# Kernel optimization log

Measured on AMD Instinct MI355X. Metric: run time of the kernel, lower is better.

The kernel has to match this reference:

```python
import jax, jax.numpy as jnp
import numpy as np

D_IN = 1024
D_OUT = 1024
SEQ = 2048
BATCH = 4


def setup_inputs() -> dict:
    key = jax.random.key(0)
    ks = jax.random.split(key, 7)
    s_in = 1.0 / np.sqrt(D_IN)
    return {
        "x": jax.random.normal(ks[0], (BATCH, SEQ, D_IN), dtype=jnp.float32),
        "Wq": jax.random.normal(ks[1], (D_IN, D_OUT), dtype=jnp.float32) * s_in,
        "bq": jax.random.normal(ks[2], (D_OUT,), dtype=jnp.float32) * 0.01,
        "Wk": jax.random.normal(ks[3], (D_IN, D_OUT), dtype=jnp.float32) * s_in,
        "bk": jax.random.normal(ks[4], (D_OUT,), dtype=jnp.float32) * 0.01,
        "Wv": jax.random.normal(ks[5], (D_IN, D_OUT), dtype=jnp.float32) * s_in,
        "bv": jax.random.normal(ks[6], (D_OUT,), dtype=jnp.float32) * 0.01,
    }


def reference(x, Wq, bq, Wk, bk, Wv, bv):
    # x: [b, n, d_in]
    b, n, d_in = x.shape
    q = x @ Wq + bq  # [b, n, d_out]
    k = x @ Wk + bk
    v = x @ Wv + bv
    scale = 1.0 / jnp.sqrt(jnp.asarray(d_in, x.dtype))
    scores = jnp.einsum("bqd,bkd->bqk", q, k) * scale  # [b, n, n]
    causal = jnp.triu(jnp.ones((n, n), dtype=bool), k=1)  # True above diagonal
    scores = jnp.where(causal, -jnp.inf, scores)
    weights = jax.nn.softmax(scores, axis=-1)
    # dropout p=0.0 -> identity
    context = jnp.einsum("bqk,bkd->bqd", weights, v)
    return context
```

## Files before the change

kernel.cpp:

```cpp
#include <hip/hip_runtime.h>

typedef unsigned short u16;
typedef __bf16 bf16x8 __attribute__((ext_vector_type(8)));
typedef float floatx4 __attribute__((ext_vector_type(4)));

#define B_ 4
#define SEQ 2048
#define DIM 1024

__device__ __forceinline__ u16 f2bf(float f) {
    unsigned u = __builtin_bit_cast(unsigned, f);
    u += 0x7FFFu + ((u >> 16) & 1u);
    return (u16)(u >> 16);
}
__device__ __forceinline__ float bf2f(u16 h) {
    unsigned u = ((unsigned)h) << 16;
    return __builtin_bit_cast(float, u);
}

#define GPTR(p) ((const __attribute__((address_space(1))) void*)(p))
#define LPTR(p) ((__attribute__((address_space(3))) void*)(p))

__global__ __launch_bounds__(256) void convert_x(const float4* __restrict__ x,
                                                 ushort4* __restrict__ xb) {
    int i = blockIdx.x * 256 + threadIdx.x;
    float4 v = x[i];
    ushort4 o;
    o.x = f2bf(v.x); o.y = f2bf(v.y); o.z = f2bf(v.z); o.w = f2bf(v.w);
    xb[i] = o;
}

__global__ __launch_bounds__(256) void transpose_w(const float* __restrict__ Wq,
                                                   const float* __restrict__ Wk,
                                                   const float* __restrict__ Wv,
                                                   u16* __restrict__ Wt) {
    __shared__ u16 t[64][66];
    const int z = blockIdx.z;
    const float* W = (z == 0) ? Wq : ((z == 1) ? Wk : Wv);
    u16* out = Wt + (size_t)z * DIM * DIM;
    const int tx = threadIdx.x, ty = threadIdx.y;
    const int k0 = blockIdx.x * 64, n0 = blockIdx.y * 64;
#pragma unroll
    for (int j = 0; j < 8; j++) {
        int k = ty + 8 * j;
        float2 v = *(const float2*)(W + (size_t)(k0 + k) * DIM + n0 + 2 * tx);
        t[2 * tx][k] = f2bf(v.x);
        t[2 * tx + 1][k] = f2bf(v.y);
    }
    __syncthreads();
#pragma unroll
    for (int j = 0; j < 8; j++) {
        int n = ty + 8 * j;
        ushort2 o;
        o.x = t[n][2 * tx];
        o.y = t[n][2 * tx + 1];
        *(ushort2*)(out + (size_t)(n0 + n) * DIM + k0 + 2 * tx) = o;
    }
}

__device__ __forceinline__ void mainloop(
    const u16* __restrict__ Ab, const u16* __restrict__ Bb, int lda, int ldb,
    int Kt, u16* lsA, u16* lsB, int tid, int wave, int quad, int l15,
    int wm, int wn, floatx4 (&acc)[4][4]) {
    const int srow = tid >> 2;
    const int scol = ((tid & 3) ^ ((tid >> 3) & 3)) * 8;
    const u16* gA = Ab + (size_t)srow * lda + scol;
    const u16* gB = Bb + (size_t)srow * ldb + scol;
    const int swq = (quad ^ ((l15 >> 1) & 3)) * 8;

#pragma unroll
    for (int i = 0; i < 4; i++)
#pragma unroll
        for (int j = 0; j < 4; j++) {
            floatx4 zz = {0.f, 0.f, 0.f, 0.f};
            acc[i][j] = zz;
        }

    for (int k0 = 0; k0 < Kt; k0 += 64) {
#pragma unroll
        for (int h = 0; h < 2; h++)
#pragma unroll
            for (int c = 0; c < 2; c++) {
                __builtin_amdgcn_global_load_lds(
                    GPTR(gA + (size_t)c * 64 * lda + h * 32),
                    LPTR(lsA + h * 4096 + c * 2048 + wave * 512), 16, 0, 0);
                __builtin_amdgcn_global_load_lds(
                    GPTR(gB + (size_t)c * 64 * ldb + h * 32),
                    LPTR(lsB + h * 4096 + c * 2048 + wave * 512), 16, 0, 0);
            }
        gA += 64; gB += 64;
        __syncthreads();

#pragma unroll
        for (int h = 0; h < 2; h++) {
            bf16x8 af[4];
#pragma unroll
            for (int i = 0; i < 4; i++)
                af[i] = *(const bf16x8*)(lsA + h * 4096 + (wm + i * 16 + l15) * 32 + swq);
#pragma unroll
            for (int j = 0; j < 4; j++) {
                bf16x8 bfr = *(const bf16x8*)(lsB + h * 4096 + (wn + j * 16 + l15) * 32 + swq);
#pragma unroll
                for (int i = 0; i < 4; i++)
                    acc[i][j] = __builtin_amdgcn_mfma_f32_16x16x32_bf16(af[i], bfr, acc[i][j], 0, 0, 0);
            }
        }
        __syncthreads();
    }
}

__global__ __launch_bounds__(256, 3) void gemm_qkv(
    const u16* __restrict__ A, const u16* __restrict__ Bt, u16* __restrict__ QK,
    const float* __restrict__ b0, const float* __restrict__ b1, const float* __restrict__ b2,
    u16* __restrict__ VtOut) {
    __shared__ union {
        struct { u16 a[128 * 64]; u16 b[128 * 64]; } stage;
        u16 epT[64 * 136];
    } sm;
    const int tid = threadIdx.x;
    const int wave = tid >> 6, lane = tid & 63;
    const int quad = lane >> 4, l15 = lane & 15;
    const int wm = (wave >> 1) * 64, wn = (wave & 1) * 64;
    const int z = blockIdx.x >> 3, xn = blockIdx.x & 7, yb = blockIdx.y;

    const u16* Ab = A + (size_t)yb * 128 * DIM;
    const u16* Bb = Bt + (size_t)z * DIM * DIM + (size_t)xn * 128 * DIM;
    floatx4 acc[4][4];
    mainloop(Ab, Bb, DIM, DIM, DIM, sm.stage.a, sm.stage.b,
             tid, wave, quad, l15, wm, wn, acc);

    const int colbase = xn * 128;
    const int mq = quad * 4;
    const float* bias = (z == 0) ? b0 : ((z == 1) ? b1 : b2);
    const int n0 = colbase + wn + l15;

    if (z < 2) {
        u16* Cb = QK + (size_t)z * B_ * SEQ * DIM;
        const int m0 = yb * 128 + wm + mq;
#pragma unroll
        for (int j = 0; j < 4; j++) {
            float bv_ = bias[n0 + j * 16];
#pragma unroll
            for (int i = 0; i < 4; i++)
#pragma unroll
                for (int r = 0; r < 4; r++)
                    Cb[(size_t)(m0 + i * 16 + r) * DIM + (n0 + j * 16)] = f2bf(acc[i][j][r] + bv_);
        }
        return;
    }

    float addj[4];
#pragma unroll
    for (int j = 0; j < 4; j++) addj[j] = bias[n0 + j * 16];
    const int b = (yb * 128) >> 11;
    const int sb = (yb * 128) & (SEQ - 1);
    u16* Vb = VtOut + (size_t)b * DIM * SEQ;
#pragma unroll
    for (int c = 0; c < 2; c++) {
        __syncthreads();
        if ((wave & 1) == c) {
#pragma unroll
            for (int i = 0; i < 4; i++)
#pragma unroll
                for (int j = 0; j < 4; j++)
#pragma unroll
                    for (int r = 0; r < 4; r++) {
                        int lr = wm + i * 16 + mq + r;
                        int lc = j * 16 + l15;
                        sm.epT[lc * 136 + lr] = f2bf(acc[i][j][r] + addj[j]);
                    }
        }
        __syncthreads();
#pragma unroll
        for (int k = 0; k < 4; k++) {
            int s2 = tid + 256 * k;
            int n = s2 >> 4, seg = s2 & 15;
            uint4 val = *(const uint4*)&sm.epT[n * 136 + seg * 8];
            *(uint4*)(Vb + (size_t)(colbase + c * 64 + n) * SEQ + sb + seg * 8) = val;
        }
    }
}

__global__ __launch_bounds__(256, 3) void gemm_scores(
    const u16* __restrict__ Q, const u16* __restrict__ K, u16* __restrict__ S,
    float scale) {
    const int ym = gridDim.y - 1 - blockIdx.y;
    if ((int)blockIdx.x > ym) return;

    __shared__ u16 lsA[128 * 64];
    __shared__ u16 lsB[128 * 64];
    const int tid = threadIdx.x;
    const int wave = tid >> 6, lane = tid & 63;
    const int quad = lane >> 4, l15 = lane & 15;
    const int wm = (wave >> 1) * 64, wn = (wave & 1) * 64;
    const int z = blockIdx.z;

    const u16* Ab = Q + (size_t)z * SEQ * DIM + (size_t)ym * 128 * DIM;
    const u16* Bb = K + (size_t)z * SEQ * DIM + (size_t)blockIdx.x * 128 * DIM;
    floatx4 acc[4][4];
    mainloop(Ab, Bb, DIM, DIM, DIM, lsA, lsB,
             tid, wave, quad, l15, wm, wn, acc);

    u16* Cb = S + (size_t)z * SEQ * SEQ;
    const int m0 = ym * 128 + wm + quad * 4;
    const int n0 = blockIdx.x * 128 + wn + l15;
#pragma unroll
    for (int j = 0; j < 4; j++)
#pragma unroll
        for (int i = 0; i < 4; i++)
#pragma unroll
            for (int r = 0; r < 4; r++)
                Cb[(size_t)(m0 + i * 16 + r) * SEQ + (n0 + j * 16)] = f2bf(acc[i][j][r] * scale);
}

__global__ __launch_bounds__(256, 3) void gemm_pv(
    const u16* __restrict__ P, const u16* __restrict__ Vt, float* __restrict__ O) {
    const int ym = gridDim.y - 1 - blockIdx.y;
    __shared__ u16 lsA[128 * 64];
    __shared__ u16 lsB[128 * 64];
    const int tid = threadIdx.x;
    const int wave = tid >> 6, lane = tid & 63;
    const int quad = lane >> 4, l15 = lane & 15;
    const int wm = (wave >> 1) * 64, wn = (wave & 1) * 64;
    const int z = blockIdx.z;

    const u16* Ab = P + (size_t)z * SEQ * SEQ + (size_t)ym * 128 * SEQ;
    const u16* Bb = Vt + (size_t)z * DIM * SEQ + (size_t)blockIdx.x * 128 * SEQ;
    const int Kt = (ym + 1) * 128;
    floatx4 acc[4][4];
    mainloop(Ab, Bb, SEQ, SEQ, Kt, lsA, lsB,
             tid, wave, quad, l15, wm, wn, acc);

    float* Cf = O + (size_t)z * SEQ * DIM;
    const int m0 = ym * 128 + wm + quad * 4;
    const int n0 = blockIdx.x * 128 + wn + l15;
#pragma unroll
    for (int j = 0; j < 4; j++)
#pragma unroll
        for (int i = 0; i < 4; i++)
#pragma unroll
            for (int r = 0; r < 4; r++)
                Cf[(size_t)(m0 + i * 16 + r) * DIM + (n0 + j * 16)] = acc[i][j][r];
}

__global__ __launch_bounds__(256) void softmax_causal(u16* __restrict__ S) {
    const int q = blockIdx.x, b = blockIdx.y, tid = threadIdx.x;
    u16* row = S + ((size_t)b * SEQ + q) * SEQ;
    const int L = q + 1;
    const int Z = ((q >> 7) + 1) << 7;
    const int k0 = tid * 8;
    __shared__ float redm[4], reds[4];

    uint4 rv = ((const uint4*)row)[tid];
    unsigned w[4] = {rv.x, rv.y, rv.z, rv.w};
    float f[8];
#pragma unroll
    for (int e = 0; e < 8; e++) {
        u16 h = (u16)((w[e >> 1] >> ((e & 1) * 16)) & 0xFFFFu);
        f[e] = (k0 + e < L) ? bf2f(h) : -3.0e38f;
    }
    float m = f[0];
#pragma unroll
    for (int e = 1; e < 8; e++) m = fmaxf(m, f[e]);
#pragma unroll
    for (int o = 32; o > 0; o >>= 1) m = fmaxf(m, __shfl_xor(m, o));
    if ((tid & 63) == 0) redm[tid >> 6] = m;
    __syncthreads();
    m = fmaxf(fmaxf(redm[0], redm[1]), fmaxf(redm[2], redm[3]));

    float p[8];
    float s = 0.f;
#pragma unroll
    for (int e = 0; e < 8; e++) {
        p[e] = (k0 + e < L) ? __expf(f[e] - m) : 0.f;
        s += p[e];
    }
#pragma unroll
    for (int o = 32; o > 0; o >>= 1) s += __shfl_xor(s, o);
    if ((tid & 63) == 0) reds[tid >> 6] = s;
    __syncthreads();
    s = reds[0] + reds[1] + reds[2] + reds[3];
    const float inv = 1.0f / s;

    if (k0 < Z) {
        unsigned o2[4];
#pragma unroll
        for (int e = 0; e < 4; e++) {
            unsigned lo = f2bf(p[2 * e] * inv);
            unsigned hi = f2bf(p[2 * e + 1] * inv);
            o2[e] = lo | (hi << 16);
        }
        uint4 ov = {o2[0], o2[1], o2[2], o2[3]};
        ((uint4*)row)[tid] = ov;
    }
}

extern "C" void kernel_launch(void* const* d_in, const int* in_sizes, int n_in,
                              void* d_out, int out_size, void* d_ws, size_t ws_size,
                              hipStream_t stream) {
    const float* x = (const float*)d_in[0];
    const float* Wq = (const float*)d_in[1];
    const float* bq = (const float*)d_in[2];
    const float* Wk = (const float*)d_in[3];
    const float* bk = (const float*)d_in[4];
    const float* Wv = (const float*)d_in[5];
    const float* bv = (const float*)d_in[6];
    float* out = (float*)d_out;

    char* ws = (char*)d_ws;
    const size_t MB = 1024ull * 1024ull;
    u16* S = (u16*)ws;
    u16* xb = (u16*)ws;
    u16* Wt = (u16*)(ws + 16 * MB);
    u16* QK = (u16*)(ws + 32 * MB);
    u16* Vt = (u16*)(ws + 64 * MB);
    const size_t MAT = (size_t)B_ * SEQ * DIM;
    u16* Q = QK;
    u16* Km = QK + MAT;

    const float scale = 0.03125f;

    convert_x<<<8192, 256, 0, stream>>>((const float4*)x, (ushort4*)xb);
    transpose_w<<<dim3(16, 16, 3), dim3(32, 8), 0, stream>>>(Wq, Wk, Wv, Wt);
    gemm_qkv<<<dim3(24, 64), 256, 0, stream>>>(xb, Wt, QK, bq, bk, bv, Vt);
    gemm_scores<<<dim3(16, 16, 4), 256, 0, stream>>>(Q, Km, S, scale);
    softmax_causal<<<dim3(SEQ, B_), 256, 0, stream>>>(S);
    gemm_pv<<<dim3(8, 16, 4), 256, 0, stream>>>(S, Vt, out);
}
```

Before: 250.7 us.

## Rewrite QKV projection GEMM with 256x256 tiles and pipelined direct-to-LDS loads

Replaces the 128x128-tile QKV GEMM with a 512-thread kernel computing 256x256 tiles. It double-buffers operands in LDS using global_load_lds, with staggered waitcnt/barrier phases so prefetch overlaps MFMA work. Workgroups are remapped so tiles sharing operands are scheduled close together, and the V transpose epilogue now uses an XOR-swizzled LDS buffer. The larger tile raises data reuse and cuts global traffic. The cost is 128KB of LDS and heavy register use, which lowers occupancy and leaves 384 blocks for the GPU's compute units.

```diff
diff --git a/kernel.cpp b/kernel.cpp
--- a/kernel.cpp
+++ b/kernel.cpp
@@ -20,6 +20,7 @@
 
 #define GPTR(p) ((const __attribute__((address_space(1))) void*)(p))
 #define LPTR(p) ((__attribute__((address_space(3))) void*)(p))
+#define GLD(src, dstp) __builtin_amdgcn_global_load_lds(GPTR(src), LPTR(dstp), 16, 0, 0)
 
 __global__ __launch_bounds__(256) void convert_x(const float4* __restrict__ x,
                                                  ushort4* __restrict__ xb) {
@@ -109,75 +110,172 @@
     }
 }
 
-__global__ __launch_bounds__(256, 3) void gemm_qkv(
+__global__ __launch_bounds__(512, 2) void gemm_qkv256(
     const u16* __restrict__ A, const u16* __restrict__ Bt, u16* __restrict__ QK,
     const float* __restrict__ b0, const float* __restrict__ b1, const float* __restrict__ b2,
     u16* __restrict__ VtOut) {
     __shared__ union {
-        struct { u16 a[128 * 64]; u16 b[128 * 64]; } stage;
-        u16 epT[64 * 136];
+        u16 stage[2][32768];
+        u16 T[65536];
     } sm;
+    u16* lsbase = &sm.stage[0][0];
+
     const int tid = threadIdx.x;
     const int wave = tid >> 6, lane = tid & 63;
     const int quad = lane >> 4, l15 = lane & 15;
-    const int wm = (wave >> 1) * 64, wn = (wave & 1) * 64;
-    const int z = blockIdx.x >> 3, xn = blockIdx.x & 7, yb = blockIdx.y;
-
-    const u16* Ab = A + (size_t)yb * 128 * DIM;
-    const u16* Bb = Bt + (size_t)z * DIM * DIM + (size_t)xn * 128 * DIM;
-    floatx4 acc[4][4];
-    mainloop(Ab, Bb, DIM, DIM, DIM, sm.stage.a, sm.stage.b,
-             tid, wave, quad, l15, wm, wn, acc);
-
-    const int colbase = xn * 128;
-    const int mq = quad * 4;
+    const int wmH = wave >> 2;
+    const int wnI = wave & 3;
+    const int swq = (quad ^ ((l15 >> 1) & 3)) * 8;
+    const int rdoff = l15 * 32 + swq;
+
+    const int bid = blockIdx.x;
+    const int wgid = (bid & 7) * 48 + (bid >> 3);
+    const int mt = wgid & 31, nt = wgid >> 5;
+
+    const int rl = (tid & 255) >> 2;
+    const int sS = tid >> 8;
+    const int sseg = ((tid & 3) ^ ((tid >> 3) & 3)) * 8;
+    const u16* sA = A + (size_t)mt * 256 * DIM + (size_t)rl * DIM + sS * 32 + sseg;
+    const u16* sB = Bt + (size_t)nt * 256 * DIM + (size_t)rl * DIM + sS * 32 + sseg;
+
+    {
+        u16* An0 = lsbase;
+        u16* Bn0 = lsbase + 16384;
+        GLD(sB,                      Bn0 + 0     + wave * 512);
+        GLD(sB + (size_t)64  * DIM,  Bn0 + 4096  + wave * 512);
+        GLD(sB + (size_t)128 * DIM,  Bn0 + 8192  + wave * 512);
+        GLD(sB + (size_t)192 * DIM,  Bn0 + 12288 + wave * 512);
+        GLD(sA,                      An0 + 0     + wave * 512);
+        GLD(sA + (size_t)128 * DIM,  An0 + 8192  + wave * 512);
+        GLD(sA + (size_t)64  * DIM,  An0 + 4096  + wave * 512);
+        GLD(sA + (size_t)192 * DIM,  An0 + 12288 + wave * 512);
+    }
+    const u16* sAk = sA + 64;
+    const u16* sBk = sB + 64;
+
+    floatx4 acc[8][4];
+#pragma unroll
+    for (int i = 0; i < 8; i++)
+#pragma unroll
+        for (int j = 0; j < 4; j++) {
+            floatx4 zz = {0.f, 0.f, 0.f, 0.f};
+            acc[i][j] = zz;
+        }
+
+    const int NT = DIM / 64;
+#pragma unroll 2
+    for (int t = 0; t < NT; ++t) {
+        const u16* Ac = lsbase + (t & 1) * 32768 + wmH * 8192;
+        const u16* Bc = lsbase + (t & 1) * 32768 + 16384 + (wnI >> 1) * 8192 + (wnI & 1) * 4096;
+        u16* An = lsbase + ((t & 1) ^ 1) * 32768;
+        u16* Bn = An + 16384;
+        const bool pf = (t + 1 < NT);
+        bf16x8 bq[4][2];
+
+#pragma unroll
+        for (int p = 0; p < 4; ++p) {
+            if (p == 0)       asm volatile("s_waitcnt vmcnt(2)" ::: "memory");
+            else if (p == 2) {
+                if (pf)       asm volatile("s_waitcnt vmcnt(4)" ::: "memory");
+                else          asm volatile("s_waitcnt vmcnt(0)" ::: "memory");
+            }
+            else if (p == 1)  asm volatile("s_waitcnt vmcnt(4)" ::: "memory");
+            else              asm volatile("s_waitcnt vmcnt(6)" ::: "memory");
+            __builtin_amdgcn_s_barrier();
+            asm volatile("" ::: "memory");
+
+            if (pf) {
+                if (p == 0) {
+                    GLD(sBk,                      Bn + 0     + wave * 512);
+                    GLD(sBk + (size_t)64  * DIM,  Bn + 4096  + wave * 512);
+                } else if (p == 1) {
+                    GLD(sBk + (size_t)128 * DIM,  Bn + 8192  + wave * 512);
+                    GLD(sBk + (size_t)192 * DIM,  Bn + 12288 + wave * 512);
+                } else if (p == 2) {
+                    GLD(sAk,                      An + 0     + wave * 512);
+                    GLD(sAk + (size_t)128 * DIM,  An + 8192  + wave * 512);
+                } else {
+                    GLD(sAk + (size_t)64  * DIM,  An + 4096  + wave * 512);
+                    GLD(sAk + (size_t)192 * DIM,  An + 12288 + wave * 512);
+                }
+            }
+
+            if (p == 0) {
+#pragma unroll
+                for (int j = 0; j < 4; ++j)
+#pragma unroll
+                    for (int s = 0; s < 2; ++s)
+                        bq[j][s] = *(const bf16x8*)(Bc + s * 2048 + j * 512 + rdoff);
+            }
+            const int i0 = 2 * p, i1 = 2 * p + 1;
+            bf16x8 a0[2], a1[2];
+#pragma unroll
+            for (int s = 0; s < 2; ++s) {
+                a0[s] = *(const bf16x8*)(Ac + (i0 >> 2) * 4096 + s * 2048 + (i0 & 3) * 512 + rdoff);
+                a1[s] = *(const bf16x8*)(Ac + (i1 >> 2) * 4096 + s * 2048 + (i1 & 3) * 512 + rdoff);
+            }
+
+            __builtin_amdgcn_s_setprio(1);
+#pragma unroll
+            for (int s = 0; s < 2; ++s)
+#pragma unroll
+                for (int j = 0; j < 4; ++j) {
+                    acc[i0][j] = __builtin_amdgcn_mfma_f32_16x16x32_bf16(a0[s], bq[j][s], acc[i0][j], 0, 0, 0);
+                    acc[i1][j] = __builtin_amdgcn_mfma_f32_16x16x32_bf16(a1[s], bq[j][s], acc[i1][j], 0, 0, 0);
+                }
+            __builtin_amdgcn_s_setprio(0);
+        }
+        if (pf) { sAk += 64; sBk += 64; }
+    }
+
+    const int z = nt >> 2;
+    const int nc = (nt & 3) * 256 + wnI * 64 + l15;
     const float* bias = (z == 0) ? b0 : ((z == 1) ? b1 : b2);
-    const int n0 = colbase + wn + l15;
 
     if (z < 2) {
         u16* Cb = QK + (size_t)z * B_ * SEQ * DIM;
-        const int m0 = yb * 128 + wm + mq;
-#pragma unroll
-        for (int j = 0; j < 4; j++) {
-            float bv_ = bias[n0 + j * 16];
-#pragma unroll
-            for (int i = 0; i < 4; i++)
-#pragma unroll
-                for (int r = 0; r < 4; r++)
-                    Cb[(size_t)(m0 + i * 16 + r) * DIM + (n0 + j * 16)] = f2bf(acc[i][j][r] + bv_);
+        const int m00 = mt * 256 + wmH * 128 + quad * 4;
+#pragma unroll
+        for (int j = 0; j < 4; ++j) {
+            float bv_ = bias[nc + j * 16];
+#pragma unroll
+            for (int i = 0; i < 8; ++i)
+#pragma unroll
+                for (int r = 0; r < 4; ++r)
+                    Cb[(size_t)(m00 + i * 16 + r) * DIM + nc + j * 16] =
+                        f2bf(acc[i][j][r] + bv_);
         }
         return;
     }
 
     float addj[4];
 #pragma unroll
-    for (int j = 0; j < 4; j++) addj[j] = bias[n0 + j * 16];
-    const int b = (yb * 128) >> 11;
-    const int sb = (yb * 128) & (SEQ - 1);
-    u16* Vb = VtOut + (size_t)b * DIM * SEQ;
-#pragma unroll
-    for (int c = 0; c < 2; c++) {
-        __syncthreads();
-        if ((wave & 1) == c) {
-#pragma unroll
-            for (int i = 0; i < 4; i++)
-#pragma unroll
-                for (int j = 0; j < 4; j++)
-#pragma unroll
-                    for (int r = 0; r < 4; r++) {
-                        int lr = wm + i * 16 + mq + r;
-                        int lc = j * 16 + l15;
-                        sm.epT[lc * 136 + lr] = f2bf(acc[i][j][r] + addj[j]);
-                    }
-        }
-        __syncthreads();
-#pragma unroll
-        for (int k = 0; k < 4; k++) {
-            int s2 = tid + 256 * k;
-            int n = s2 >> 4, seg = s2 & 15;
-            uint4 val = *(const uint4*)&sm.epT[n * 136 + seg * 8];
-            *(uint4*)(Vb + (size_t)(colbase + c * 64 + n) * SEQ + sb + seg * 8) = val;
-        }
+    for (int j = 0; j < 4; ++j) addj[j] = bias[nc + j * 16];
+    __syncthreads();
+#pragma unroll
+    for (int i = 0; i < 8; ++i) {
+        const int tb = wmH * 128 + i * 16 + quad * 4;
+#pragma unroll
+        for (int j = 0; j < 4; ++j) {
+            const int d = wnI * 64 + j * 16 + l15;
+            ushort4 o;
+            o.x = f2bf(acc[i][j][0] + addj[j]);
+            o.y = f2bf(acc[i][j][1] + addj[j]);
+            o.z = f2bf(acc[i][j][2] + addj[j]);
+            o.w = f2bf(acc[i][j][3] + addj[j]);
+            *(ushort4*)&sm.T[d * 256 + (tb ^ ((d & 7) << 3))] = o;
+        }
+    }
+    __syncthreads();
+    const int bI = mt >> 3;
+    const int sbase = (mt & 7) * 256;
+    u16* Vb = VtOut + (size_t)bI * DIM * SEQ + (size_t)(nt - 8) * 256 * SEQ + sbase;
+#pragma unroll
+    for (int k = 0; k < 16; ++k) {
+        int idx = tid + 512 * k;
+        int d = idx >> 5, sg = idx & 31;
+        uint4 v = *(const uint4*)&sm.T[d * 256 + ((sg * 8) ^ ((d & 7) << 3))];
+        *(uint4*)(Vb + (size_t)d * SEQ + sg * 8) = v;
     }
 }
 
@@ -322,7 +420,7 @@
 
     convert_x<<<8192, 256, 0, stream>>>((const float4*)x, (ushort4*)xb);
     transpose_w<<<dim3(16, 16, 3), dim3(32, 8), 0, stream>>>(Wq, Wk, Wv, Wt);
-    gemm_qkv<<<dim3(24, 64), 256, 0, stream>>>(xb, Wt, QK, bq, bk, bv, Vt);
+    gemm_qkv256<<<dim3(384), dim3(512), 0, stream>>>(xb, Wt, QK, bq, bk, bv, Vt);
     gemm_scores<<<dim3(16, 16, 4), 256, 0, stream>>>(Q, Km, S, scale);
     softmax_causal<<<dim3(SEQ, B_), 256, 0, stream>>>(S);
     gemm_pv<<<dim3(8, 16, 4), 256, 0, stream>>>(S, Vt, out);
```

Result: no change. 255.0 us (+1.7%).

## Rewrite QKV GEMM with 4-stage LDS ring, 256x128 tiles and XCD-aware block mapping

Applied to the files above, without the earlier changes.

Replaces the QKV projection GEMM with a 512-thread kernel using 256x128 tiles and a 4-deep ring of LDS stages filled by global_load_lds. It double-buffers register fragments and overlaps loads with MFMA under explicit waitcnt and priority control. Block IDs are remapped so consecutive blocks land on the same XCD for L2 reuse, and the V transpose epilogue goes through a swizzled shared tile written as wider vectors. The aim is to hide memory latency and cut per-tile overhead in the largest GEMM. In exchange it takes more LDS and registers, which limits occupancy, and relies on hand-tuned synchronisation.

```diff
diff --git a/kernel.cpp b/kernel.cpp
--- a/kernel.cpp
+++ b/kernel.cpp
@@ -20,6 +20,7 @@
 
 #define GPTR(p) ((const __attribute__((address_space(1))) void*)(p))
 #define LPTR(p) ((__attribute__((address_space(3))) void*)(p))
+#define GLD(src, dstp) __builtin_amdgcn_global_load_lds(GPTR(src), LPTR(dstp), 16, 0, 0)
 
 __global__ __launch_bounds__(256) void convert_x(const float4* __restrict__ x,
                                                  ushort4* __restrict__ xb) {
@@ -109,75 +110,152 @@
     }
 }
 
-__global__ __launch_bounds__(256, 3) void gemm_qkv(
+struct Frag { bf16x8 a[4]; bf16x8 b[4]; };
+
+__global__ __launch_bounds__(512, 2) void gemm_qkv_ring(
     const u16* __restrict__ A, const u16* __restrict__ Bt, u16* __restrict__ QK,
     const float* __restrict__ b0, const float* __restrict__ b1, const float* __restrict__ b2,
     u16* __restrict__ VtOut) {
     __shared__ union {
-        struct { u16 a[128 * 64]; u16 b[128 * 64]; } stage;
-        u16 epT[64 * 136];
+        u16 stage[4][12288];
+        u16 T[128 * 256];
     } sm;
+    u16* stg = &sm.stage[0][0];
+
     const int tid = threadIdx.x;
     const int wave = tid >> 6, lane = tid & 63;
     const int quad = lane >> 4, l15 = lane & 15;
-    const int wm = (wave >> 1) * 64, wn = (wave & 1) * 64;
-    const int z = blockIdx.x >> 3, xn = blockIdx.x & 7, yb = blockIdx.y;
-
-    const u16* Ab = A + (size_t)yb * 128 * DIM;
-    const u16* Bb = Bt + (size_t)z * DIM * DIM + (size_t)xn * 128 * DIM;
+    const int wmQ = wave >> 1;
+    const int wnH = wave & 1;
+    const int swq = (quad ^ ((l15 >> 1) & 3)) * 8;
+    const int raOff = wmQ * 2048 + l15 * 32 + swq;
+    const int rbOff = 8192 + wnH * 2048 + l15 * 32 + swq;
+
+    const int bid = blockIdx.x;
+    const int wgid = (bid & 7) * 96 + (bid >> 3);
+    const int mt = wgid / 24, nt = wgid % 24;
+
+    const int srow = tid >> 2;
+    const int sseg = ((tid & 3) ^ ((tid >> 3) & 3)) * 8;
+    const u16* sAk = A + (size_t)(mt * 256 + srow) * DIM + sseg;
+    const u16* sBk = Bt + (size_t)(nt * 128 + srow) * DIM + sseg;
+    const int wl = wave * 512;
+
+#pragma unroll
+    for (int X = 0; X < 3; ++X) {
+        u16* d = stg + X * 12288;
+        GLD(sAk + X * 32,                      d + wl);
+        GLD(sAk + X * 32 + (size_t)128 * DIM,  d + 4096 + wl);
+        GLD(sBk + X * 32,                      d + 8192 + wl);
+    }
+    sAk += 96; sBk += 96;
+
     floatx4 acc[4][4];
-    mainloop(Ab, Bb, DIM, DIM, DIM, sm.stage.a, sm.stage.b,
-             tid, wave, quad, l15, wm, wn, acc);
-
-    const int colbase = xn * 128;
-    const int mq = quad * 4;
+#pragma unroll
+    for (int i = 0; i < 4; i++)
+#pragma unroll
+        for (int j = 0; j < 4; j++) {
+            floatx4 zz = {0.f, 0.f, 0.f, 0.f};
+            acc[i][j] = zz;
+        }
+
+    Frag F0, F1;
+    asm volatile("s_waitcnt vmcnt(6)" ::: "memory");
+    __builtin_amdgcn_s_barrier();
+    {
+        const u16* bufN = stg;
+#pragma unroll
+        for (int i = 0; i < 4; ++i) F0.a[i] = *(const bf16x8*)(bufN + raOff + i * 512);
+#pragma unroll
+        for (int j = 0; j < 4; ++j) F0.b[j] = *(const bf16x8*)(bufN + rbOff + j * 512);
+    }
+
+    auto phase = [&](int T, Frag& CUR, Frag& NXT) {
+        if (T <= 28) {
+            u16* d = stg + ((T + 3) & 3) * 12288;
+            GLD(sAk,                      d + wl);
+            GLD(sAk + (size_t)128 * DIM,  d + 4096 + wl);
+            GLD(sBk,                      d + 8192 + wl);
+            sAk += 32; sBk += 32;
+        }
+        if (T < 31) {
+            if (T <= 28)      asm volatile("s_waitcnt vmcnt(6)" ::: "memory");
+            else if (T == 29) asm volatile("s_waitcnt vmcnt(3)" ::: "memory");
+            else              asm volatile("s_waitcnt vmcnt(0)" ::: "memory");
+            __builtin_amdgcn_s_barrier();
+            const u16* bufN = stg + ((T + 1) & 3) * 12288;
+#pragma unroll
+            for (int i = 0; i < 4; ++i) NXT.a[i] = *(const bf16x8*)(bufN + raOff + i * 512);
+#pragma unroll
+            for (int j = 0; j < 4; ++j) NXT.b[j] = *(const bf16x8*)(bufN + rbOff + j * 512);
+            asm volatile("s_waitcnt lgkmcnt(8)" ::: "memory");
+        } else {
+            asm volatile("s_waitcnt lgkmcnt(0)" ::: "memory");
+        }
+        __builtin_amdgcn_sched_barrier(0);
+        __builtin_amdgcn_s_setprio(1);
+#pragma unroll
+        for (int j = 0; j < 4; ++j)
+#pragma unroll
+            for (int i = 0; i < 4; ++i)
+                acc[i][j] = __builtin_amdgcn_mfma_f32_16x16x32_bf16(CUR.a[i], CUR.b[j], acc[i][j], 0, 0, 0);
+        __builtin_amdgcn_s_setprio(0);
+        __builtin_amdgcn_sched_barrier(0);
+        __builtin_amdgcn_s_barrier();
+    };
+
+    for (int T = 0; T < 32; T += 2) {
+        phase(T, F0, F1);
+        phase(T + 1, F1, F0);
+    }
+
+    const int z = nt >> 3;
+    const int nc = (nt & 7) * 128 + wnH * 64 + l15;
     const float* bias = (z == 0) ? b0 : ((z == 1) ? b1 : b2);
-    const int n0 = colbase + wn + l15;
 
     if (z < 2) {
         u16* Cb = QK + (size_t)z * B_ * SEQ * DIM;
-        const int m0 = yb * 128 + wm + mq;
-#pragma unroll
-        for (int j = 0; j < 4; j++) {
-            float bv_ = bias[n0 + j * 16];
-#pragma unroll
-            for (int i = 0; i < 4; i++)
-#pragma unroll
-                for (int r = 0; r < 4; r++)
-                    Cb[(size_t)(m0 + i * 16 + r) * DIM + (n0 + j * 16)] = f2bf(acc[i][j][r] + bv_);
+        const int m00 = mt * 256 + wmQ * 64 + quad * 4;
+#pragma unroll
+        for (int j = 0; j < 4; ++j) {
+            float bv_ = bias[nc + j * 16];
+#pragma unroll
+            for (int i = 0; i < 4; ++i)
+#pragma unroll
+                for (int r = 0; r < 4; ++r)
+                    Cb[(size_t)(m00 + i * 16 + r) * DIM + nc + j * 16] =
+                        f2bf(acc[i][j][r] + bv_);
         }
         return;
     }
 
     float addj[4];
 #pragma unroll
-    for (int j = 0; j < 4; j++) addj[j] = bias[n0 + j * 16];
-    const int b = (yb * 128) >> 11;
-    const int sb = (yb * 128) & (SEQ - 1);
-    u16* Vb = VtOut + (size_t)b * DIM * SEQ;
-#pragma unroll
-    for (int c = 0; c < 2; c++) {
-        __syncthreads();
-        if ((wave & 1) == c) {
-#pragma unroll
-            for (int i = 0; i < 4; i++)
-#pragma unroll
-                for (int j = 0; j < 4; j++)
-#pragma unroll
-                    for (int r = 0; r < 4; r++) {
-                        int lr = wm + i * 16 + mq + r;
-                        int lc = j * 16 + l15;
-                        sm.epT[lc * 136 + lr] = f2bf(acc[i][j][r] + addj[j]);
-                    }
-        }
-        __syncthreads();
-#pragma unroll
-        for (int k = 0; k < 4; k++) {
-            int s2 = tid + 256 * k;
-            int n = s2 >> 4, seg = s2 & 15;
-            uint4 val = *(const uint4*)&sm.epT[n * 136 + seg * 8];
-            *(uint4*)(Vb + (size_t)(colbase + c * 64 + n) * SEQ + sb + seg * 8) = val;
-        }
+    for (int j = 0; j < 4; ++j) addj[j] = bias[nc + j * 16];
+#pragma unroll
+    for (int i = 0; i < 4; ++i) {
+        const int tb = wmQ * 64 + i * 16 + quad * 4;
+#pragma unroll
+        for (int j = 0; j < 4; ++j) {
+            const int d = wnH * 64 + j * 16 + l15;
+            ushort4 o;
+            o.x = f2bf(acc[i][j][0] + addj[j]);
+            o.y = f2bf(acc[i][j][1] + addj[j]);
+            o.z = f2bf(acc[i][j][2] + addj[j]);
+            o.w = f2bf(acc[i][j][3] + addj[j]);
+            *(ushort4*)&sm.T[d * 256 + (tb ^ ((d & 7) << 3))] = o;
+        }
+    }
+    __syncthreads();
+    const int bI = mt >> 3;
+    const int sbase = (mt & 7) * 256;
+    u16* Vb = VtOut + (size_t)bI * DIM * SEQ + (size_t)(nt - 16) * 128 * SEQ + sbase;
+#pragma unroll
+    for (int k = 0; k < 8; ++k) {
+        int idx = tid + 512 * k;
+        int d = idx >> 5, sg = idx & 31;
+        uint4 v = *(const uint4*)&sm.T[d * 256 + ((sg * 8) ^ ((d & 7) << 3))];
+        *(uint4*)(Vb + (size_t)d * SEQ + sg * 8) = v;
     }
 }
 
@@ -322,7 +400,7 @@
 
     convert_x<<<8192, 256, 0, stream>>>((const float4*)x, (ushort4*)xb);
     transpose_w<<<dim3(16, 16, 3), dim3(32, 8), 0, stream>>>(Wq, Wk, Wv, Wt);
-    gemm_qkv<<<dim3(24, 64), 256, 0, stream>>>(xb, Wt, QK, bq, bk, bv, Vt);
+    gemm_qkv_ring<<<dim3(768), dim3(512), 0, stream>>>(xb, Wt, QK, bq, bk, bv, Vt);
     gemm_scores<<<dim3(16, 16, 4), 256, 0, stream>>>(Q, Km, S, scale);
     softmax_causal<<<dim3(SEQ, B_), 256, 0, stream>>>(S);
     gemm_pv<<<dim3(8, 16, 4), 256, 0, stream>>>(S, Vt, out);
```

After: 261.0 us. 4.1% more time.

## Rewrite QKV projection GEMM with 128x256 tiles and triple-buffered direct-to-LDS loads

Applied to the files above, without the earlier changes.

Replaces the QKV projection GEMM with a 512-thread kernel using 128x256 output tiles, a three-stage LDS ring filled by global_load_lds with XOR swizzling, explicit vmcnt waits and MFMA priority bumps. The 1D grid is remapped so consecutive blocks are spread across XCD-like groups, and the V transpose epilogue uses a swizzled full-tile LDS buffer. It aims to hide global load latency and raise data reuse per block. In exchange it uses much more LDS per block (about 144KB), which limits occupancy, and relies on hand-tuned wait counts.

```diff
diff --git a/kernel.cpp b/kernel.cpp
--- a/kernel.cpp
+++ b/kernel.cpp
@@ -20,6 +20,7 @@
 
 #define GPTR(p) ((const __attribute__((address_space(1))) void*)(p))
 #define LPTR(p) ((__attribute__((address_space(3))) void*)(p))
+#define GLD(src, dstp) __builtin_amdgcn_global_load_lds(GPTR(src), LPTR(dstp), 16, 0, 0)
 
 __global__ __launch_bounds__(256) void convert_x(const float4* __restrict__ x,
                                                  ushort4* __restrict__ xb) {
@@ -109,75 +110,146 @@
     }
 }
 
-__global__ __launch_bounds__(256, 3) void gemm_qkv(
+__global__ __launch_bounds__(512, 2) void gemm_qkv_r3(
     const u16* __restrict__ A, const u16* __restrict__ Bt, u16* __restrict__ QK,
-    const float* __restrict__ b0, const float* __restrict__ b1, const float* __restrict__ b2,
-    u16* __restrict__ VtOut) {
+    const float* __restrict__ b0, const float* __restrict__ b1,
+    const float* __restrict__ b2, u16* __restrict__ VtOut) {
     __shared__ union {
-        struct { u16 a[128 * 64]; u16 b[128 * 64]; } stage;
-        u16 epT[64 * 136];
+        u16 stage[3][24576];
+        u16 T[256 * 128];
     } sm;
+
     const int tid = threadIdx.x;
     const int wave = tid >> 6, lane = tid & 63;
     const int quad = lane >> 4, l15 = lane & 15;
-    const int wm = (wave >> 1) * 64, wn = (wave & 1) * 64;
-    const int z = blockIdx.x >> 3, xn = blockIdx.x & 7, yb = blockIdx.y;
-
-    const u16* Ab = A + (size_t)yb * 128 * DIM;
-    const u16* Bb = Bt + (size_t)z * DIM * DIM + (size_t)xn * 128 * DIM;
+    const int wm = (wave >> 2) * 64;
+    const int wn = (wave & 3) * 64;
+    const int wl = wave * 512;
+
+    const int bid = blockIdx.x;
+    const int wgid = (bid & 7) * 96 + (bid >> 3);
+    const int mt = wgid & 63, nt = wgid >> 6;
+
+    const int srow = tid >> 3;
+    const int sseg = (tid & 7) ^ (srow & 7);
+    const u16* gA = A + (size_t)(mt * 128 + srow) * DIM + sseg * 8;
+    const u16* gB = Bt + (size_t)(nt * 256 + srow) * DIM + sseg * 8;
+
+    u16* p0 = &sm.stage[0][0];
+    u16* p1 = &sm.stage[1][0];
+    u16* p2 = &sm.stage[2][0];
+
+    const int s0 = (quad ^ (l15 & 7)) * 8;
+    const int rAoff = (wm + l15) * 64;
+    const int rBoff = 8192 + (wn + l15) * 64;
+
     floatx4 acc[4][4];
-    mainloop(Ab, Bb, DIM, DIM, DIM, sm.stage.a, sm.stage.b,
-             tid, wave, quad, l15, wm, wn, acc);
-
-    const int colbase = xn * 128;
-    const int mq = quad * 4;
+#pragma unroll
+    for (int i = 0; i < 4; i++)
+#pragma unroll
+        for (int j = 0; j < 4; j++) {
+            floatx4 zz = {0.f, 0.f, 0.f, 0.f};
+            acc[i][j] = zz;
+        }
+
+#define QKV_STAGE(bW) do { \
+    GLD(gA,                      (bW) + wl); \
+    GLD(gA + (size_t)64 * DIM,   (bW) + 4096 + wl); \
+    GLD(gB,                      (bW) + 8192 + wl); \
+    GLD(gB + (size_t)64 * DIM,   (bW) + 12288 + wl); \
+    GLD(gB + (size_t)128 * DIM,  (bW) + 16384 + wl); \
+    GLD(gB + (size_t)192 * DIM,  (bW) + 20480 + wl); \
+    gA += 64; gB += 64; } while (0)
+
+#define QKV_TILE(bR, bW, STG, EVM) do { \
+    __builtin_amdgcn_s_barrier(); \
+    if (STG) QKV_STAGE(bW); \
+    const u16* rA_ = (bR) + rAoff; \
+    const u16* rB_ = (bR) + rBoff; \
+    bf16x8 a_[4], bv_[4]; \
+    _Pragma("unroll") for (int i_ = 0; i_ < 4; ++i_) a_[i_] = *(const bf16x8*)(rA_ + i_ * 1024 + s0); \
+    _Pragma("unroll") for (int j_ = 0; j_ < 4; ++j_) bv_[j_] = *(const bf16x8*)(rB_ + j_ * 1024 + s0); \
+    __builtin_amdgcn_s_setprio(1); \
+    _Pragma("unroll") for (int j_ = 0; j_ < 4; ++j_) \
+    _Pragma("unroll") for (int i_ = 0; i_ < 4; ++i_) \
+        acc[i_][j_] = __builtin_amdgcn_mfma_f32_16x16x32_bf16(a_[i_], bv_[j_], acc[i_][j_], 0, 0, 0); \
+    __builtin_amdgcn_s_setprio(0); \
+    _Pragma("unroll") for (int i_ = 0; i_ < 4; ++i_) a_[i_] = *(const bf16x8*)(rA_ + i_ * 1024 + (s0 ^ 32)); \
+    _Pragma("unroll") for (int j_ = 0; j_ < 4; ++j_) bv_[j_] = *(const bf16x8*)(rB_ + j_ * 1024 + (s0 ^ 32)); \
+    __builtin_amdgcn_s_setprio(1); \
+    _Pragma("unroll") for (int j_ = 0; j_ < 4; ++j_) \
+    _Pragma("unroll") for (int i_ = 0; i_ < 4; ++i_) \
+        acc[i_][j_] = __builtin_amdgcn_mfma_f32_16x16x32_bf16(a_[i_], bv_[j_], acc[i_][j_], 0, 0, 0); \
+    __builtin_amdgcn_s_setprio(0); \
+    if ((EVM) == 6) { asm volatile("s_waitcnt vmcnt(6)" ::: "memory"); } \
+    else if ((EVM) == 0) { asm volatile("s_waitcnt vmcnt(0)" ::: "memory"); } \
+    } while (0)
+
+    QKV_STAGE(p0);
+    QKV_STAGE(p1);
+    asm volatile("s_waitcnt vmcnt(6)" ::: "memory");
+
+    for (int tt = 0; tt < 4; ++tt) {
+        QKV_TILE(p0, p2, 1, 6);
+        QKV_TILE(p1, p0, 1, 6);
+        QKV_TILE(p2, p1, 1, 6);
+    }
+    QKV_TILE(p0, p2, 1, 6);
+    QKV_TILE(p1, p0, 1, 6);
+    QKV_TILE(p2, p1, 0, 0);
+    QKV_TILE(p0, p1, 0, -1);
+
+#undef QKV_TILE
+#undef QKV_STAGE
+
+    const int z = nt >> 2;
+    const int nc = (nt & 3) * 256 + wn + l15;
     const float* bias = (z == 0) ? b0 : ((z == 1) ? b1 : b2);
-    const int n0 = colbase + wn + l15;
 
     if (z < 2) {
         u16* Cb = QK + (size_t)z * B_ * SEQ * DIM;
-        const int m0 = yb * 128 + wm + mq;
-#pragma unroll
-        for (int j = 0; j < 4; j++) {
-            float bv_ = bias[n0 + j * 16];
-#pragma unroll
-            for (int i = 0; i < 4; i++)
-#pragma unroll
-                for (int r = 0; r < 4; r++)
-                    Cb[(size_t)(m0 + i * 16 + r) * DIM + (n0 + j * 16)] = f2bf(acc[i][j][r] + bv_);
+        const int m00 = mt * 128 + wm + quad * 4;
+#pragma unroll
+        for (int j = 0; j < 4; ++j) {
+            float bv2 = bias[nc + j * 16];
+#pragma unroll
+            for (int i = 0; i < 4; ++i)
+#pragma unroll
+                for (int r = 0; r < 4; ++r)
+                    Cb[(size_t)(m00 + i * 16 + r) * DIM + nc + j * 16] =
+                        f2bf(acc[i][j][r] + bv2);
         }
         return;
     }
 
     float addj[4];
 #pragma unroll
-    for (int j = 0; j < 4; j++) addj[j] = bias[n0 + j * 16];
-    const int b = (yb * 128) >> 11;
-    const int sb = (yb * 128) & (SEQ - 1);
-    u16* Vb = VtOut + (size_t)b * DIM * SEQ;
-#pragma unroll
-    for (int c = 0; c < 2; c++) {
-        __syncthreads();
-        if ((wave & 1) == c) {
-#pragma unroll
-            for (int i = 0; i < 4; i++)
-#pragma unroll
-                for (int j = 0; j < 4; j++)
-#pragma unroll
-                    for (int r = 0; r < 4; r++) {
-                        int lr = wm + i * 16 + mq + r;
-                        int lc = j * 16 + l15;
-                        sm.epT[lc * 136 + lr] = f2bf(acc[i][j][r] + addj[j]);
-                    }
-        }
-        __syncthreads();
-#pragma unroll
-        for (int k = 0; k < 4; k++) {
-            int s2 = tid + 256 * k;
-            int n = s2 >> 4, seg = s2 & 15;
-            uint4 val = *(const uint4*)&sm.epT[n * 136 + seg * 8];
-            *(uint4*)(Vb + (size_t)(colbase + c * 64 + n) * SEQ + sb + seg * 8) = val;
-        }
+    for (int j = 0; j < 4; ++j) addj[j] = bias[nc + j * 16];
+    __syncthreads();
+#pragma unroll
+    for (int i = 0; i < 4; ++i) {
+        const int tb = wm + i * 16 + quad * 4;
+#pragma unroll
+        for (int j = 0; j < 4; ++j) {
+            const int d = wn + j * 16 + l15;
+            ushort4 o;
+            o.x = f2bf(acc[i][j][0] + addj[j]);
+            o.y = f2bf(acc[i][j][1] + addj[j]);
+            o.z = f2bf(acc[i][j][2] + addj[j]);
+            o.w = f2bf(acc[i][j][3] + addj[j]);
+            *(ushort4*)&sm.T[d * 128 + (tb ^ ((d & 7) << 3))] = o;
+        }
+    }
+    __syncthreads();
+    const int bI = mt >> 4;
+    const int sbase = (mt & 15) * 128;
+    u16* Vb = VtOut + (size_t)bI * DIM * SEQ + (size_t)(nt - 8) * 256 * SEQ + sbase;
+#pragma unroll
+    for (int k = 0; k < 8; ++k) {
+        int idx = tid + 512 * k;
+        int d = idx >> 4, sg = idx & 15;
+        uint4 v = *(const uint4*)&sm.T[d * 128 + ((sg * 8) ^ ((d & 7) << 3))];
+        *(uint4*)(Vb + (size_t)d * SEQ + sg * 8) = v;
     }
 }
 
@@ -322,7 +394,7 @@
 
     convert_x<<<8192, 256, 0, stream>>>((const float4*)x, (ushort4*)xb);
     transpose_w<<<dim3(16, 16, 3), dim3(32, 8), 0, stream>>>(Wq, Wk, Wv, Wt);
-    gemm_qkv<<<dim3(24, 64), 256, 0, stream>>>(xb, Wt, QK, bq, bk, bv, Vt);
+    gemm_qkv_r3<<<dim3(768), dim3(512), 0, stream>>>(xb, Wt, QK, bq, bk, bv, Vt);
     gemm_scores<<<dim3(16, 16, 4), 256, 0, stream>>>(Q, Km, S, scale);
     softmax_causal<<<dim3(SEQ, B_), 256, 0, stream>>>(S);
     gemm_pv<<<dim3(8, 16, 4), 256, 0, stream>>>(S, Vt, out);
```

After: 253.7 us. No clear change (+1.2%).
